# Kernel optimization log

Hardware: AMD Instinct MI355X
Metric: run time of the kernel (lower is better)

The kernel has to match this reference:

```python
import jax, jax.numpy as jnp
import numpy as np

GROUP = 64          # quantization group size along input dim
EPS = 1e-6          # rms_norm_eps
THETA = 1000000.0   # rope theta
NUM_HEADS = 16
NUM_KV_HEADS = 4
HEAD_DIM = 128


def _qlinear(x, wq, s, b=None):
    # dequantize int8-valued weights with per-group scales, then GEMM
    o, i = wq.shape
    w = (wq.reshape(o, i // GROUP, GROUP).astype(jnp.float32) * s[:, :, None]).reshape(o, i)
    y = jnp.einsum('bsi,oi->bso', x, w)
    return y + b if b is not None else y


def _rmsnorm(x, w):
    return x * jax.lax.rsqrt(jnp.mean(x * x, axis=-1, keepdims=True) + EPS) * w


def _rope(x, offset):
    # x: [B, H, S, hd], neox-style half rotation
    hd = x.shape[-1]
    S = x.shape[2]
    pos = (jnp.arange(S) + offset).astype(jnp.float32)
    inv = THETA ** (-(jnp.arange(0, hd, 2).astype(jnp.float32)) / hd)  # [hd/2]
    ang = pos[:, None] * inv[None, :]                                  # [S, hd/2]
    cos, sin = jnp.cos(ang), jnp.sin(ang)
    x1, x2 = x[..., : hd // 2], x[..., hd // 2 :]
    return jnp.concatenate([x1 * cos - x2 * sin, x2 * cos + x1 * sin], axis=-1)


def setup_inputs() -> dict:
    key = jax.random.key(0)
    B, S, D, I = 2, 1024, 2048, 5632
    KV = NUM_KV_HEADS * HEAD_DIM  # 512
    keys = iter(jax.random.split(key, 32))

    def qw(shape):
        return jax.random.randint(next(keys), shape, -127, 128, dtype=jnp.int32)

    def sc(shape):
        return jax.random.uniform(next(keys), shape, jnp.float32, 0.5, 1.5) * 0.001

    inp = {
        'x': jax.random.normal(next(keys), (B, S, D), jnp.float32),
        'wq_q': qw((D, D)),   'wq_s': sc((D, D // GROUP)),
        'bq': jax.random.normal(next(keys), (D,), jnp.float32) * 0.02,
        'wk_q': qw((KV, D)),  'wk_s': sc((KV, D // GROUP)),
        'bk': jax.random.normal(next(keys), (KV,), jnp.float32) * 0.02,
        'wv_q': qw((KV, D)),  'wv_s': sc((KV, D // GROUP)),
        'bv': jax.random.normal(next(keys), (KV,), jnp.float32) * 0.02,
        'wo_q': qw((D, D)),   'wo_s': sc((D, D // GROUP)),
        'gate_q': qw((I, D)), 'gate_s': sc((I, D // GROUP)),
        'up_q': qw((I, D)),   'up_s': sc((I, D // GROUP)),
        'down_q': qw((D, I)), 'down_s': sc((D, I // GROUP)),
        'w_in_ln': jnp.ones((D,), jnp.float32),
        'w_post_ln': jnp.ones((D,), jnp.float32),
        'offset': 0,
    }
    return inp


def reference(x, wq_q, wq_s, bq, wk_q, wk_s, bk, wv_q, wv_s, bv, wo_q, wo_s,
              gate_q, gate_s, up_q, up_s, down_q, down_s, w_in_ln, w_post_ln, offset):
    B, S, D = x.shape
    H, KVH, hd = NUM_HEADS, NUM_KV_HEADS, HEAD_DIM

    # --- attention sub-block ---
    h = _rmsnorm(x, w_in_ln)
    q = _qlinear(h, wq_q, wq_s, bq).reshape(B, S, H, hd).transpose(0, 2, 1, 3)
    k = _qlinear(h, wk_q, wk_s, bk).reshape(B, S, KVH, hd).transpose(0, 2, 1, 3)
    v = _qlinear(h, wv_q, wv_s, bv).reshape(B, S, KVH, hd).transpose(0, 2, 1, 3)
    q = _rope(q, offset)
    k = _rope(k, offset)

    g = H // KVH  # query groups per kv head
    qg = q.reshape(B, KVH, g, S, hd)
    scores = jnp.einsum('bghsd,bgtd->bghst', qg, k) * (1.0 / np.sqrt(hd)).astype(np.float32)
    causal = jnp.tril(jnp.ones((S, S), dtype=bool))  # prefill causal mask (empty cache)
    scores = jnp.where(causal, scores, jnp.float32(-1e9))
    p = jax.nn.softmax(scores, axis=-1)
    o = jnp.einsum('bghst,bgtd->bghsd', p, v)
    o = o.reshape(B, H, S, hd).transpose(0, 2, 1, 3).reshape(B, S, D)
    x = x + _qlinear(o, wo_q, wo_s)

    # --- mlp sub-block ---
    h2 = _rmsnorm(x, w_post_ln)
    gate = jax.nn.silu(_qlinear(h2, gate_q, gate_s))
    up = _qlinear(h2, up_q, up_s)
    mlp = _qlinear(gate * up, down_q, down_s)
    return x + mlp
```

## Files before the change

### kernel.cpp

```cpp
#include <hip/hip_runtime.h>
#include <cstdint>
#include <cstddef>

#define DEV __device__ __forceinline__

typedef _Float16 f16x8 __attribute__((ext_vector_type(8)));
typedef float f32x4 __attribute__((ext_vector_type(4)));

static constexpr int D_MODEL = 2048;
static constexpr int D_FF    = 5632;
static constexpr int N_QKV   = 3072;
static constexpr int SEQ     = 1024;
static constexpr int BATCH   = 2;
static constexpr int ROWS    = BATCH * SEQ;
static constexpr int HEADS   = 16;
static constexpr int HD      = 128;

DEV uint16_t f2h(float f) {
    return __builtin_bit_cast(uint16_t, (_Float16)f);
}
DEV float h2f(uint16_t u) {
    return (float)__builtin_bit_cast(_Float16, u);
}

DEV void async_load16(const void* g, void* lds) {
    __builtin_amdgcn_global_load_lds(
        reinterpret_cast<__attribute__((address_space(1))) void*>(
            reinterpret_cast<uintptr_t>(g)),
        reinterpret_cast<__attribute__((address_space(3))) void*>(
            static_cast<uint32_t>(reinterpret_cast<uintptr_t>(lds))),
        16, 0, 0);
}

__global__ __launch_bounds__(256)
void dequant_kernel(const int* __restrict__ q, const float* __restrict__ s,
                    uint16_t* __restrict__ wout, int n4, int I, int mode)
{
    const int idx = blockIdx.x * 256 + threadIdx.x;
    if (idx >= n4) return;
    const int e = idx * 4;
    const int row = e / I;
    const int i = e - row * I;
    const int4 qv = *reinterpret_cast<const int4*>(&q[e]);
    const float scf = s[row * (I >> 6) + (i >> 6)];
    int orow = row;
    if (mode == 1) orow = ((row >> 4) << 5) + (row & 15);
    else if (mode == 2) orow = ((row >> 4) << 5) + (row & 15) + 16;
    uint16_t h[4];
    h[0] = f2h((float)qv.x * scf);
    h[1] = f2h((float)qv.y * scf);
    h[2] = f2h((float)qv.z * scf);
    h[3] = f2h((float)qv.w * scf);
    uint2 pk;
    pk.x = (uint32_t)h[0] | ((uint32_t)h[1] << 16);
    pk.y = (uint32_t)h[2] | ((uint32_t)h[3] << 16);
    *reinterpret_cast<uint2*>(&wout[(size_t)orow * I + i]) = pk;
}

__global__ __launch_bounds__(256)
void biascat_kernel(const float* __restrict__ bq, const float* __restrict__ bk,
                    const float* __restrict__ bv, float* __restrict__ out)
{
    const int i = blockIdx.x * 256 + threadIdx.x;
    if (i >= N_QKV) return;
    float v;
    if (i < 2048)      v = bq[i];
    else if (i < 2560) v = bk[i - 2048];
    else               v = bv[i - 2560];
    out[i] = v;
}

__global__ __launch_bounds__(256)
void rmsnorm_kernel(const float* __restrict__ x, const float* __restrict__ wln,
                    uint16_t* __restrict__ out)
{
    __shared__ float red[4];
    const int row = blockIdx.x;
    const int tid = threadIdx.x;
    const float* xr = x + (size_t)row * D_MODEL;
    const float4 v0 = *reinterpret_cast<const float4*>(&xr[tid * 8]);
    const float4 v1 = *reinterpret_cast<const float4*>(&xr[tid * 8 + 4]);
    float ss = v0.x*v0.x + v0.y*v0.y + v0.z*v0.z + v0.w*v0.w
             + v1.x*v1.x + v1.y*v1.y + v1.z*v1.z + v1.w*v1.w;
#pragma unroll
    for (int off = 32; off; off >>= 1) ss += __shfl_xor(ss, off);
    if ((tid & 63) == 0) red[tid >> 6] = ss;
    __syncthreads();
    const float rms = rsqrtf((red[0] + red[1] + red[2] + red[3]) * (1.0f / D_MODEL) + 1e-6f);
    const int cb = tid * 8;
    const size_t base = (size_t)row * D_MODEL + cb;
    const float vals[8] = {v0.x, v0.y, v0.z, v0.w, v1.x, v1.y, v1.z, v1.w};
#pragma unroll
    for (int k = 0; k < 8; k += 2) {
        const uint16_t h0 = f2h(vals[k] * rms * wln[cb + k]);
        const uint16_t h1 = f2h(vals[k + 1] * rms * wln[cb + k + 1]);
        *reinterpret_cast<uint32_t*>(&out[base + k]) = (uint32_t)h0 | ((uint32_t)h1 << 16);
    }
}

__global__ __launch_bounds__(256)
void gemm_f16_glu_kernel(const uint16_t* __restrict__ A, const uint16_t* __restrict__ W,
                         uint16_t* __restrict__ outh, int M, int N, int K)
{
    __shared__ uint16_t sA[2][128 * 64];
    __shared__ uint16_t sB[2][128 * 64];

    const int tid  = threadIdx.x;
    const int lane = tid & 63;
    const int wv   = tid >> 6;
    const int wm   = wv >> 1;
    const int wn   = wv & 1;
    const int quad = lane >> 4;
    const int l16  = lane & 15;

    const int nBn = N >> 7;
    const int bm  = blockIdx.x / nBn;
    const int bn  = blockIdx.x - bm * nBn;
    const int m0  = bm << 7;
    const int n0  = bn << 7;

    f32x4 acc[4][4];
#pragma unroll
    for (int i = 0; i < 4; i++)
#pragma unroll
        for (int j = 0; j < 4; j++)
            acc[i][j] = (f32x4){0.f, 0.f, 0.f, 0.f};

    const uint16_t* Ab = A + (size_t)m0 * K;
    const uint16_t* Wb = W + (size_t)n0 * K;

    auto stage = [&](int kt, int bsel) {
#pragma unroll
        for (int p = 0; p < 4; p++) {
            const int cb = p * 256 + wv * 64;
            const int c  = cb + lane;
            const int row = c >> 3;
            const int g   = (c & 7) ^ (row & 7);
            const size_t goff = (size_t)row * K + kt + g * 8;
            async_load16(Ab + goff, &sA[bsel][cb * 8]);
            async_load16(Wb + goff, &sB[bsel][cb * 8]);
        }
    };

    stage(0, 0);
    __syncthreads();

    const int nKt = K >> 6;
    for (int t = 0; t < nKt; t++) {
        const int cur = t & 1;
        if (t + 1 < nKt) stage((t + 1) << 6, cur ^ 1);
        const uint16_t* sAc = sA[cur];
        const uint16_t* sBc = sB[cur];
#pragma unroll
        for (int kk = 0; kk < 2; kk++) {
            const int gsw = ((kk * 4 + quad) ^ (l16 & 7)) * 8;
            f16x8 bfv[4];
#pragma unroll
            for (int j = 0; j < 4; j++)
                bfv[j] = *reinterpret_cast<const f16x8*>(
                    &sBc[(wn * 64 + j * 16 + l16) * 64 + gsw]);
#pragma unroll
            for (int i = 0; i < 4; i++) {
                const f16x8 af = *reinterpret_cast<const f16x8*>(
                    &sAc[(wm * 64 + i * 16 + l16) * 64 + gsw]);
#pragma unroll
                for (int j = 0; j < 4; j++)
                    acc[i][j] = __builtin_amdgcn_mfma_f32_16x16x32_f16(af, bfv[j], acc[i][j], 0, 0, 0);
            }
        }
        __syncthreads();
    }

    const int NH = N >> 1;
#pragma unroll
    for (int i = 0; i < 4; i++) {
        const int rowb = m0 + wm * 64 + i * 16 + quad * 4;
#pragma unroll
        for (int r = 0; r < 4; r++) {
            const size_t rr = (size_t)(rowb + r);
#pragma unroll
            for (int pjt = 0; pjt < 2; pjt++) {
                const float g = acc[i][2 * pjt][r];
                const float u = acc[i][2 * pjt + 1][r];
                const float a = (g / (1.0f + __expf(-g))) * u;
                const int cc = (n0 >> 1) + wn * 32 + pjt * 16 + l16;
                outh[rr * NH + cc] = f2h(a);
            }
        }
    }
}

__global__ __launch_bounds__(256)
void gemm_f16_m64_kernel(const uint16_t* __restrict__ A, const uint16_t* __restrict__ W,
                         const float* __restrict__ bias, const float* __restrict__ resid,
                         float* __restrict__ outf, int M, int N, int K)
{
    __shared__ uint16_t sA[2][64 * 64];
    __shared__ uint16_t sB[2][128 * 64];

    const int tid  = threadIdx.x;
    const int lane = tid & 63;
    const int wv   = tid >> 6;
    const int quad = lane >> 4;
    const int l16  = lane & 15;

    const int nBn = N >> 7;
    const int bm  = blockIdx.x / nBn;
    const int bn  = blockIdx.x - bm * nBn;
    const int m0  = bm << 6;
    const int n0  = bn << 7;

    f32x4 acc[4][2];
#pragma unroll
    for (int i = 0; i < 4; i++)
#pragma unroll
        for (int j = 0; j < 2; j++)
            acc[i][j] = (f32x4){0.f, 0.f, 0.f, 0.f};

    const uint16_t* Ab = A + (size_t)m0 * K;
    const uint16_t* Wb = W + (size_t)n0 * K;

    auto stage = [&](int kt, int bsel) {
#pragma unroll
        for (int p = 0; p < 2; p++) {
            const int cb = p * 256 + wv * 64;
            const int c  = cb + lane;
            const int row = c >> 3;
            const int g   = (c & 7) ^ (row & 7);
            async_load16(Ab + (size_t)row * K + kt + g * 8, &sA[bsel][cb * 8]);
        }
#pragma unroll
        for (int p = 0; p < 4; p++) {
            const int cb = p * 256 + wv * 64;
            const int c  = cb + lane;
            const int row = c >> 3;
            const int g   = (c & 7) ^ (row & 7);
            async_load16(Wb + (size_t)row * K + kt + g * 8, &sB[bsel][cb * 8]);
        }
    };

    stage(0, 0);
    __syncthreads();

    const int nKt = K >> 6;
    for (int t = 0; t < nKt; t++) {
        const int cur = t & 1;
        if (t + 1 < nKt) stage((t + 1) << 6, cur ^ 1);
        const uint16_t* sAc = sA[cur];
        const uint16_t* sBc = sB[cur];
#pragma unroll
        for (int kk = 0; kk < 2; kk++) {
            const int gsw = ((kk * 4 + quad) ^ (l16 & 7)) * 8;
            f16x8 bfv[2];
#pragma unroll
            for (int j = 0; j < 2; j++)
                bfv[j] = *reinterpret_cast<const f16x8*>(
                    &sBc[(wv * 32 + j * 16 + l16) * 64 + gsw]);
#pragma unroll
            for (int i = 0; i < 4; i++) {
                const f16x8 af = *reinterpret_cast<const f16x8*>(
                    &sAc[(i * 16 + l16) * 64 + gsw]);
#pragma unroll
                for (int j = 0; j < 2; j++)
                    acc[i][j] = __builtin_amdgcn_mfma_f32_16x16x32_f16(af, bfv[j], acc[i][j], 0, 0, 0);
            }
        }
        __syncthreads();
    }

#pragma unroll
    for (int i = 0; i < 4; i++) {
        const int rowb = m0 + i * 16 + quad * 4;
#pragma unroll
        for (int r = 0; r < 4; r++) {
            const size_t rr = (size_t)(rowb + r);
#pragma unroll
            for (int j = 0; j < 2; j++) {
                const int cc = n0 + wv * 32 + j * 16 + l16;
                float v = acc[i][j][r];
                if (bias)  v += bias[cc];
                if (resid) v += resid[rr * N + cc];
                outf[rr * N + cc] = v;
            }
        }
    }
}

__global__ __launch_bounds__(256)
void rope_q_kernel(const float* __restrict__ qkv, const int* __restrict__ offp,
                   uint16_t* __restrict__ Qb)
{
    const int idx = blockIdx.x * 256 + threadIdx.x;
    const int d   = idx & 63;
    const int h   = (idx >> 6) & 15;
    const int row = idx >> 10;
    const int b   = row >> 10;
    const int s   = row & (SEQ - 1);
    const float pos  = (float)(s + *offp);
    const float freq = powf(1.0e6f, -(float)d * (1.0f / 64.0f));
    float sn, cs;
    sincosf(pos * freq, &sn, &cs);
    const size_t gb = (size_t)row * N_QKV + h * HD + d;
    const float x1 = qkv[gb];
    const float x2 = qkv[gb + 64];
    const float qscale = 0.08838834764831845f;
    const size_t ob = ((size_t)(b * 16 + h) * SEQ + s) * HD + d;
    Qb[ob]      = f2h((x1 * cs - x2 * sn) * qscale);
    Qb[ob + 64] = f2h((x2 * cs + x1 * sn) * qscale);
}

__global__ __launch_bounds__(256)
void rope_k_kernel(const float* __restrict__ qkv, const int* __restrict__ offp,
                   uint16_t* __restrict__ Kb)
{
    const int idx = blockIdx.x * 256 + threadIdx.x;
    const int d   = idx & 63;
    const int kvh = (idx >> 6) & 3;
    const int row = idx >> 8;
    const int b   = row >> 10;
    const int s   = row & (SEQ - 1);
    const float pos  = (float)(s + *offp);
    const float freq = powf(1.0e6f, -(float)d * (1.0f / 64.0f));
    float sn, cs;
    sincosf(pos * freq, &sn, &cs);
    const size_t gb = (size_t)row * N_QKV + 2048 + kvh * HD + d;
    const float x1 = qkv[gb];
    const float x2 = qkv[gb + 64];
    const size_t ob = ((size_t)(b * 4 + kvh) * SEQ + s) * HD + d;
    Kb[ob]      = f2h(x1 * cs - x2 * sn);
    Kb[ob + 64] = f2h(x2 * cs + x1 * sn);
}

__global__ __launch_bounds__(256)
void prep_v_kernel(const float* __restrict__ qkv, uint16_t* __restrict__ Vt)
{
    __shared__ uint16_t sh[128 * 72];
    const int tid = threadIdx.x;
    const int sc  = blockIdx.x & 15;
    const int bk  = blockIdx.x >> 4;
    const int b   = bk >> 2, kvh = bk & 3;
#pragma unroll
    for (int p = 0; p < 8; p++) {
        const int q4 = p * 256 + tid;
        const int sloc = q4 >> 5, d4 = (q4 & 31) * 4;
        const float4 v = *reinterpret_cast<const float4*>(
            &qkv[(size_t)(b * SEQ + sc * 64 + sloc) * N_QKV + 2560 + kvh * HD + d4]);
        sh[(d4 + 0) * 72 + sloc] = f2h(v.x);
        sh[(d4 + 1) * 72 + sloc] = f2h(v.y);
        sh[(d4 + 2) * 72 + sloc] = f2h(v.z);
        sh[(d4 + 3) * 72 + sloc] = f2h(v.w);
    }
    __syncthreads();
    const int d = tid >> 1, half = tid & 1;
    const size_t ob = ((size_t)(bk * 128 + d)) * SEQ + sc * 64 + half * 32;
    const uint16_t* srh = &sh[d * 72 + half * 32];
#pragma unroll
    for (int k = 0; k < 4; k++)
        *reinterpret_cast<uint4*>(&Vt[ob + k * 8]) =
            *reinterpret_cast<const uint4*>(&srh[k * 8]);
}

__global__ __launch_bounds__(256)
void attn_kernel(const uint16_t* __restrict__ Qb, const uint16_t* __restrict__ Kb,
                 const uint16_t* __restrict__ Vt, uint16_t* __restrict__ att)
{
    __shared__ uint16_t sK[2][32 * 128];
    __shared__ uint16_t sV[2][128 * 32];
    __shared__ uint16_t sP[4 * 16 * 32];

    const int tid  = threadIdx.x;
    const int lane = tid & 63;
    const int wv   = tid >> 6;
    const int quad = lane >> 4;
    const int l16  = lane & 15;
    const int qsw  = (quad ^ ((l16 >> 1) & 3)) * 8;

    const int bi  = blockIdx.x;
    const int sc  = 15 - (bi >> 5);
    const int bh  = bi & 31;
    const int b   = bh >> 4;
    const int h   = bh & 15;
    const int kvh = h >> 2;
    const int s0  = sc << 6;

    f16x8 qf[4];
    {
        const size_t qb = ((size_t)(b * 16 + h) * SEQ + s0 + wv * 16 + l16) * HD;
#pragma unroll
        for (int ks = 0; ks < 4; ks++)
            qf[ks] = *reinterpret_cast<const f16x8*>(&Qb[qb + ks * 32 + quad * 8]);
    }

    float m_i[4], l_i[4];
#pragma unroll
    for (int r = 0; r < 4; r++) { m_i[r] = -1e30f; l_i[r] = 0.f; }
    f32x4 oacc[8];
#pragma unroll
    for (int dt = 0; dt < 8; dt++) oacc[dt] = (f32x4){0.f, 0.f, 0.f, 0.f};

    const size_t kb = (size_t)(b * 4 + kvh) * SEQ * HD;
    const size_t vb = (size_t)(b * 4 + kvh) * HD * SEQ;

    auto stageKV = [&](int t0, int bsel) {
#pragma unroll
        for (int p = 0; p < 2; p++) {
            const int cb = p * 256 + wv * 64;
            const int c  = cb + lane;
            const int krow = c >> 4;
            const int kcc  = (c & 15) ^ (krow & 7);
            async_load16(Kb + kb + (size_t)(t0 + krow) * HD + kcc * 8, &sK[bsel][cb * 8]);
            const int vrow = c >> 2;
            const int vcc  = (c & 3) ^ ((vrow >> 1) & 3);
            async_load16(Vt + vb + (size_t)vrow * SEQ + t0 + vcc * 8, &sV[bsel][cb * 8]);
        }
    };

    const int ntiles = 2 * sc + 2;
    stageKV(0, 0);
    __syncthreads();

    for (int tt = 0; tt < ntiles; tt++) {
        const int t0 = tt << 5;
        const int cur = tt & 1;
        if (tt + 1 < ntiles) stageKV((tt + 1) << 5, cur ^ 1);

        f32x4 sacc[2];
        sacc[0] = (f32x4){0.f, 0.f, 0.f, 0.f};
        sacc[1] = (f32x4){0.f, 0.f, 0.f, 0.f};
#pragma unroll
        for (int ks = 0; ks < 4; ks++) {
#pragma unroll
            for (int jt = 0; jt < 2; jt++) {
                const int idx = (jt * 16 + l16) * 128 + (((ks * 4 + quad) ^ (l16 & 7)) * 8);
                const f16x8 kf = *reinterpret_cast<const f16x8*>(&sK[cur][idx]);
                sacc[jt] = __builtin_amdgcn_mfma_f32_16x16x32_f16(qf[ks], kf, sacc[jt], 0, 0, 0);
            }
        }

        if (t0 >= s0) {
            const int rowg = s0 + wv * 16 + quad * 4;
#pragma unroll
            for (int jt = 0; jt < 2; jt++) {
                const int key = t0 + jt * 16 + l16;
#pragma unroll
                for (int r = 0; r < 4; r++)
                    if (key > rowg + r) sacc[jt][r] = -1e30f;
            }
        }

        float alpha[4];
#pragma unroll
        for (int r = 0; r < 4; r++) {
            float mt = fmaxf(sacc[0][r], sacc[1][r]);
#pragma unroll
            for (int off = 8; off; off >>= 1) mt = fmaxf(mt, __shfl_xor(mt, off));
            const float mn = fmaxf(m_i[r], mt);
            alpha[r] = __expf(m_i[r] - mn);
            const float p0 = __expf(sacc[0][r] - mn);
            const float p1 = __expf(sacc[1][r] - mn);
            float ps = p0 + p1;
#pragma unroll
            for (int off = 8; off; off >>= 1) ps += __shfl_xor(ps, off);
            l_i[r] = l_i[r] * alpha[r] + ps;
            m_i[r] = mn;
            const int prow = quad * 4 + r;
            sP[wv * 512 + prow * 32 + 0 * 16 + l16] = f2h(p0);
            sP[wv * 512 + prow * 32 + 1 * 16 + l16] = f2h(p1);
        }

#pragma unroll
        for (int dt = 0; dt < 8; dt++) {
#pragma unroll
            for (int r = 0; r < 4; r++) oacc[dt][r] *= alpha[r];
        }
        const f16x8 pf = *reinterpret_cast<const f16x8*>(&sP[wv * 512 + l16 * 32 + quad * 8]);
#pragma unroll
        for (int dt = 0; dt < 8; dt++) {
            const f16x8 vf = *reinterpret_cast<const f16x8*>(&sV[cur][(dt * 16 + l16) * 32 + qsw]);
            oacc[dt] = __builtin_amdgcn_mfma_f32_16x16x32_f16(pf, vf, oacc[dt], 0, 0, 0);
        }

        __syncthreads();
    }

    float inv[4];
#pragma unroll
    for (int r = 0; r < 4; r++) inv[r] = 1.0f / l_i[r];
#pragma unroll
    for (int r = 0; r < 4; r++) {
        const size_t rowg = (size_t)(b * SEQ + s0 + wv * 16 + quad * 4 + r);
#pragma unroll
        for (int dt = 0; dt < 8; dt++)
            att[rowg * D_MODEL + h * HD + dt * 16 + l16] = f2h(oacc[dt][r] * inv[r]);
    }
}

extern "C" void kernel_launch(void* const* d_in, const int* in_sizes, int n_in,
                              void* d_out, int out_size, void* d_ws, size_t ws_size,
                              hipStream_t stream)
{
    (void)in_sizes; (void)n_in; (void)out_size; (void)ws_size;
    const float* x      = (const float*)d_in[0];
    const int*   wq_q   = (const int*)d_in[1];
    const float* wq_s   = (const float*)d_in[2];
    const float* bq     = (const float*)d_in[3];
    const int*   wk_q   = (const int*)d_in[4];
    const float* wk_s   = (const float*)d_in[5];
    const float* bk     = (const float*)d_in[6];
    const int*   wv_q   = (const int*)d_in[7];
    const float* wv_s   = (const float*)d_in[8];
    const float* bv     = (const float*)d_in[9];
    const int*   wo_q   = (const int*)d_in[10];
    const float* wo_s   = (const float*)d_in[11];
    const int*   gate_q = (const int*)d_in[12];
    const float* gate_s = (const float*)d_in[13];
    const int*   up_q   = (const int*)d_in[14];
    const float* up_s   = (const float*)d_in[15];
    const int*   down_q = (const int*)d_in[16];
    const float* down_s = (const float*)d_in[17];
    const float* w_in   = (const float*)d_in[18];
    const float* w_post = (const float*)d_in[19];
    const int*   offp   = (const int*)d_in[20];

    char* p = (char*)d_ws;
    auto alloc = [&](size_t bytes) {
        char* r = p;
        p += (bytes + 255) & ~(size_t)255;
        return r;
    };
    uint16_t* Wgu   = (uint16_t*)alloc((size_t)2 * D_FF * D_MODEL * 2);
    uint16_t* Wdown = (uint16_t*)alloc((size_t)D_MODEL * D_FF * 2);
    uint16_t* hbuf  = (uint16_t*)alloc((size_t)ROWS * D_MODEL * 2);
    float*    x2    = (float*)alloc((size_t)ROWS * D_MODEL * 4);
    float*    bqkv  = (float*)alloc((size_t)N_QKV * 4);
    char* zone = alloc((size_t)N_QKV * D_MODEL * 2 +
                       (size_t)D_MODEL * D_MODEL * 2 +
                       (size_t)ROWS * N_QKV * 4 + 8192);
    uint16_t* Wqkv = (uint16_t*)zone;
    uint16_t* Wo   = Wqkv + (size_t)N_QKV * D_MODEL;
    float*    qkv  = (float*)(Wo + (size_t)D_MODEL * D_MODEL);
    uint16_t* Qb = Wqkv;
    uint16_t* Kb = Qb + (size_t)BATCH * 16 * SEQ * HD;
    uint16_t* Vt = Kb + (size_t)BATCH * 4 * SEQ * HD;
    uint16_t* att = (uint16_t*)qkv;
    uint16_t* act = (uint16_t*)zone;

    auto dq = [&](const int* q, const float* s, uint16_t* o,
                  size_t n, int I, int mode) {
        const int n4 = (int)(n / 4);
        dequant_kernel<<<(n4 + 255) / 256, 256, 0, stream>>>(q, s, o, n4, I, mode);
    };
    dq(wq_q, wq_s, Wqkv, (size_t)2048 * 2048, 2048, 0);
    dq(wk_q, wk_s, Wqkv + (size_t)2048 * 2048, (size_t)512 * 2048, 2048, 0);
    dq(wv_q, wv_s, Wqkv + (size_t)2560 * 2048, (size_t)512 * 2048, 2048, 0);
    dq(wo_q, wo_s, Wo, (size_t)2048 * 2048, 2048, 0);
    dq(gate_q, gate_s, Wgu, (size_t)D_FF * 2048, 2048, 1);
    dq(up_q, up_s, Wgu, (size_t)D_FF * 2048, 2048, 2);
    dq(down_q, down_s, Wdown, (size_t)2048 * D_FF, D_FF, 0);

    biascat_kernel<<<(N_QKV + 255) / 256, 256, 0, stream>>>(bq, bk, bv, bqkv);
    rmsnorm_kernel<<<ROWS, 256, 0, stream>>>(x, w_in, hbuf);

    gemm_f16_m64_kernel<<<(ROWS / 64) * (N_QKV / 128), 256, 0, stream>>>(
        hbuf, Wqkv, bqkv, nullptr, qkv, ROWS, N_QKV, D_MODEL);

    rope_q_kernel<<<(ROWS * 16 * 64) / 256, 256, 0, stream>>>(qkv, offp, Qb);
    rope_k_kernel<<<(ROWS * 4 * 64) / 256, 256, 0, stream>>>(qkv, offp, Kb);
    prep_v_kernel<<<BATCH * 4 * (SEQ / 64), 256, 0, stream>>>(qkv, Vt);

    attn_kernel<<<BATCH * HEADS * (SEQ / 64), 256, 0, stream>>>(Qb, Kb, Vt, att);

    gemm_f16_m64_kernel<<<(ROWS / 64) * (D_MODEL / 128), 256, 0, stream>>>(
        att, Wo, nullptr, x, x2, ROWS, D_MODEL, D_MODEL);

    rmsnorm_kernel<<<ROWS, 256, 0, stream>>>(x2, w_post, hbuf);

    gemm_f16_glu_kernel<<<(ROWS / 128) * (2 * D_FF / 128), 256, 0, stream>>>(
        hbuf, Wgu, act, ROWS, 2 * D_FF, D_MODEL);

    gemm_f16_m64_kernel<<<(ROWS / 64) * (D_MODEL / 128), 256, 0, stream>>>(
        act, Wdown, nullptr, x2, (float*)d_out, ROWS, D_MODEL, D_FF);
}
```

Baseline: 569.6 us.

## Load GEMM A fragments directly from global memory and remap blocks across XCDs

Result: slower. 906.0 us (+59.1%).

```diff
diff --git a/kernel.cpp b/kernel.cpp
--- a/kernel.cpp
+++ b/kernel.cpp
@@ -98,11 +98,17 @@
     }
 }
 
+DEV void xcd_remap(int bid, int nwg, int nBm, int& bm, int& bn) {
+    const int cpx = nwg >> 3;
+    const int wg  = (bid & 7) * cpx + (bid >> 3);
+    bm = wg % nBm;
+    bn = wg / nBm;
+}
+
 __global__ __launch_bounds__(256)
 void gemm_f16_glu_kernel(const uint16_t* __restrict__ A, const uint16_t* __restrict__ W,
                          uint16_t* __restrict__ outh, int M, int N, int K)
 {
-    __shared__ uint16_t sA[2][128 * 64];
     __shared__ uint16_t sB[2][128 * 64];
 
     const int tid  = threadIdx.x;
@@ -113,9 +119,8 @@
     const int quad = lane >> 4;
     const int l16  = lane & 15;
 
-    const int nBn = N >> 7;
-    const int bm  = blockIdx.x / nBn;
-    const int bn  = blockIdx.x - bm * nBn;
+    int bm, bn;
+    xcd_remap(blockIdx.x, gridDim.x, M >> 7, bm, bn);
     const int m0  = bm << 7;
     const int n0  = bn << 7;
 
@@ -126,7 +131,7 @@
         for (int j = 0; j < 4; j++)
             acc[i][j] = (f32x4){0.f, 0.f, 0.f, 0.f};
 
-    const uint16_t* Ab = A + (size_t)m0 * K;
+    const uint16_t* Aw = A + (size_t)(m0 + wm * 64 + l16) * K;
     const uint16_t* Wb = W + (size_t)n0 * K;
 
     auto stage = [&](int kt, int bsel) {
@@ -136,9 +141,7 @@
             const int c  = cb + lane;
             const int row = c >> 3;
             const int g   = (c & 7) ^ (row & 7);
-            const size_t goff = (size_t)row * K + kt + g * 8;
-            async_load16(Ab + goff, &sA[bsel][cb * 8]);
-            async_load16(Wb + goff, &sB[bsel][cb * 8]);
+            async_load16(Wb + (size_t)row * K + kt + g * 8, &sB[bsel][cb * 8]);
         }
     };
 
@@ -148,8 +151,8 @@
     const int nKt = K >> 6;
     for (int t = 0; t < nKt; t++) {
         const int cur = t & 1;
-        if (t + 1 < nKt) stage((t + 1) << 6, cur ^ 1);
-        const uint16_t* sAc = sA[cur];
+        const int kt  = t << 6;
+        if (t + 1 < nKt) stage(kt + 64, cur ^ 1);
         const uint16_t* sBc = sB[cur];
 #pragma unroll
         for (int kk = 0; kk < 2; kk++) {
@@ -162,7 +165,7 @@
 #pragma unroll
             for (int i = 0; i < 4; i++) {
                 const f16x8 af = *reinterpret_cast<const f16x8*>(
-                    &sAc[(wm * 64 + i * 16 + l16) * 64 + gsw]);
+                    &Aw[(size_t)(i * 16) * K + kt + kk * 32 + quad * 8]);
 #pragma unroll
                 for (int j = 0; j < 4; j++)
                     acc[i][j] = __builtin_amdgcn_mfma_f32_16x16x32_f16(af, bfv[j], acc[i][j], 0, 0, 0);
@@ -195,7 +198,6 @@
                          const float* __restrict__ bias, const float* __restrict__ resid,
                          float* __restrict__ outf, int M, int N, int K)
 {
-    __shared__ uint16_t sA[2][64 * 64];
     __shared__ uint16_t sB[2][128 * 64];
 
     const int tid  = threadIdx.x;
@@ -204,9 +206,8 @@
     const int quad = lane >> 4;
     const int l16  = lane & 15;
 
-    const int nBn = N >> 7;
-    const int bm  = blockIdx.x / nBn;
-    const int bn  = blockIdx.x - bm * nBn;
+    int bm, bn;
+    xcd_remap(blockIdx.x, gridDim.x, M >> 6, bm, bn);
     const int m0  = bm << 6;
     const int n0  = bn << 7;
 
@@ -217,18 +218,10 @@
         for (int j = 0; j < 2; j++)
             acc[i][j] = (f32x4){0.f, 0.f, 0.f, 0.f};
 
-    const uint16_t* Ab = A + (size_t)m0 * K;
+    const uint16_t* Aw = A + (size_t)(m0 + l16) * K;
     const uint16_t* Wb = W + (size_t)n0 * K;
 
     auto stage = [&](int kt, int bsel) {
-#pragma unroll
-        for (int p = 0; p < 2; p++) {
-            const int cb = p * 256 + wv * 64;
-            const int c  = cb + lane;
-            const int row = c >> 3;
-            const int g   = (c & 7) ^ (row & 7);
-            async_load16(Ab + (size_t)row * K + kt + g * 8, &sA[bsel][cb * 8]);
-        }
 #pragma unroll
         for (int p = 0; p < 4; p++) {
             const int cb = p * 256 + wv * 64;
@@ -245,8 +238,8 @@
     const int nKt = K >> 6;
     for (int t = 0; t < nKt; t++) {
         const int cur = t & 1;
-        if (t + 1 < nKt) stage((t + 1) << 6, cur ^ 1);
-        const uint16_t* sAc = sA[cur];
+        const int kt  = t << 6;
+        if (t + 1 < nKt) stage(kt + 64, cur ^ 1);
         const uint16_t* sBc = sB[cur];
 #pragma unroll
         for (int kk = 0; kk < 2; kk++) {
@@ -259,7 +252,7 @@
 #pragma unroll
             for (int i = 0; i < 4; i++) {
                 const f16x8 af = *reinterpret_cast<const f16x8*>(
-                    &sAc[(i * 16 + l16) * 64 + gsw]);
+                    &Aw[(size_t)(i * 16) * K + kt + kk * 32 + quad * 8]);
 #pragma unroll
                 for (int j = 0; j < 2; j++)
                     acc[i][j] = __builtin_amdgcn_mfma_f32_16x16x32_f16(af, bfv[j], acc[i][j], 0, 0, 0);
```

## Merge dequant launches, fold bias concat into GEMM, fuse rope, add XCD remap

Applied to the files above, without the earlier changes.

Result: faster. 558.3 us (-2.0%).

```diff
diff --git a/kernel.cpp b/kernel.cpp
--- a/kernel.cpp
+++ b/kernel.cpp
@@ -19,9 +19,6 @@
 DEV uint16_t f2h(float f) {
     return __builtin_bit_cast(uint16_t, (_Float16)f);
 }
-DEV float h2f(uint16_t u) {
-    return (float)__builtin_bit_cast(_Float16, u);
-}
 
 DEV void async_load16(const void* g, void* lds) {
     __builtin_amdgcn_global_load_lds(
@@ -32,12 +29,30 @@
         16, 0, 0);
 }
 
-__global__ __launch_bounds__(256)
-void dequant_kernel(const int* __restrict__ q, const float* __restrict__ s,
-                    uint16_t* __restrict__ wout, int n4, int I, int mode)
-{
-    const int idx = blockIdx.x * 256 + threadIdx.x;
-    if (idx >= n4) return;
+static constexpr int DQ_BLOCKS = 44032;
+
+__global__ __launch_bounds__(256)
+void dequant_all_kernel(const int* __restrict__ wq_q, const float* __restrict__ wq_s,
+                        const int* __restrict__ wk_q, const float* __restrict__ wk_s,
+                        const int* __restrict__ wv_q, const float* __restrict__ wv_s,
+                        const int* __restrict__ wo_q, const float* __restrict__ wo_s,
+                        const int* __restrict__ gate_q, const float* __restrict__ gate_s,
+                        const int* __restrict__ up_q, const float* __restrict__ up_s,
+                        const int* __restrict__ down_q, const float* __restrict__ down_s,
+                        uint16_t* __restrict__ Wqkv, uint16_t* __restrict__ Wo,
+                        uint16_t* __restrict__ Wgu, uint16_t* __restrict__ Wdown)
+{
+    const int bid = blockIdx.x;
+    const int* q; const float* s; uint16_t* out; int I, mode, seg0;
+    if (bid < 4096)        { q = wq_q;   s = wq_s;   out = Wqkv;                      I = 2048; mode = 0; seg0 = 0; }
+    else if (bid < 5120)   { q = wk_q;   s = wk_s;   out = Wqkv + 2048 * 2048;        I = 2048; mode = 0; seg0 = 4096; }
+    else if (bid < 6144)   { q = wv_q;   s = wv_s;   out = Wqkv + 2560 * 2048;        I = 2048; mode = 0; seg0 = 5120; }
+    else if (bid < 10240)  { q = wo_q;   s = wo_s;   out = Wo;                        I = 2048; mode = 0; seg0 = 6144; }
+    else if (bid < 21504)  { q = gate_q; s = gate_s; out = Wgu;                       I = 2048; mode = 1; seg0 = 10240; }
+    else if (bid < 32768)  { q = up_q;   s = up_s;   out = Wgu;                       I = 2048; mode = 2; seg0 = 21504; }
+    else                   { q = down_q; s = down_s; out = Wdown;                     I = 5632; mode = 0; seg0 = 32768; }
+
+    const int idx = (bid - seg0) * 256 + threadIdx.x;
     const int e = idx * 4;
     const int row = e / I;
     const int i = e - row * I;
@@ -54,20 +69,7 @@
     uint2 pk;
     pk.x = (uint32_t)h[0] | ((uint32_t)h[1] << 16);
     pk.y = (uint32_t)h[2] | ((uint32_t)h[3] << 16);
-    *reinterpret_cast<uint2*>(&wout[(size_t)orow * I + i]) = pk;
-}
-
-__global__ __launch_bounds__(256)
-void biascat_kernel(const float* __restrict__ bq, const float* __restrict__ bk,
-                    const float* __restrict__ bv, float* __restrict__ out)
-{
-    const int i = blockIdx.x * 256 + threadIdx.x;
-    if (i >= N_QKV) return;
-    float v;
-    if (i < 2048)      v = bq[i];
-    else if (i < 2560) v = bk[i - 2048];
-    else               v = bv[i - 2560];
-    out[i] = v;
+    *reinterpret_cast<uint2*>(&out[(size_t)orow * I + i]) = pk;
 }
 
 __global__ __launch_bounds__(256)
@@ -98,6 +100,13 @@
     }
 }
 
+DEV void xcd_remap(int bid, int nwg, int nBm, int& bm, int& bn) {
+    const int cpx = nwg >> 3;
+    const int wg  = (bid & 7) * cpx + (bid >> 3);
+    bm = wg % nBm;
+    bn = wg / nBm;
+}
+
 __global__ __launch_bounds__(256)
 void gemm_f16_glu_kernel(const uint16_t* __restrict__ A, const uint16_t* __restrict__ W,
                          uint16_t* __restrict__ outh, int M, int N, int K)
@@ -113,9 +122,8 @@
     const int quad = lane >> 4;
     const int l16  = lane & 15;
 
-    const int nBn = N >> 7;
-    const int bm  = blockIdx.x / nBn;
-    const int bn  = blockIdx.x - bm * nBn;
+    int bm, bn;
+    xcd_remap(blockIdx.x, gridDim.x, M >> 7, bm, bn);
     const int m0  = bm << 7;
     const int n0  = bn << 7;
 
@@ -192,7 +200,8 @@
 
 __global__ __launch_bounds__(256)
 void gemm_f16_m64_kernel(const uint16_t* __restrict__ A, const uint16_t* __restrict__ W,
-                         const float* __restrict__ bias, const float* __restrict__ resid,
+                         const float* __restrict__ bq, const float* __restrict__ bk,
+                         const float* __restrict__ bv, const float* __restrict__ resid,
                          float* __restrict__ outf, int M, int N, int K)
 {
     __shared__ uint16_t sA[2][64 * 64];
@@ -204,9 +213,8 @@
     const int quad = lane >> 4;
     const int l16  = lane & 15;
 
-    const int nBn = N >> 7;
-    const int bm  = blockIdx.x / nBn;
-    const int bn  = blockIdx.x - bm * nBn;
+    int bm, bn;
+    xcd_remap(blockIdx.x, gridDim.x, M >> 6, bm, bn);
     const int m0  = bm << 6;
     const int n0  = bn << 7;
 
@@ -278,7 +286,13 @@
             for (int j = 0; j < 2; j++) {
                 const int cc = n0 + wv * 32 + j * 16 + l16;
                 float v = acc[i][j][r];
-                if (bias)  v += bias[cc];
+                if (bq) {
+                    float bb;
+                    if (cc < 2048)      bb = bq[cc];
+                    else if (cc < 2560) bb = bk[cc - 2048];
+                    else                bb = bv[cc - 2560];
+                    v += bb;
+                }
                 if (resid) v += resid[rr * N + cc];
                 outf[rr * N + cc] = v;
             }
@@ -286,49 +300,50 @@
     }
 }
 
-__global__ __launch_bounds__(256)
-void rope_q_kernel(const float* __restrict__ qkv, const int* __restrict__ offp,
-                   uint16_t* __restrict__ Qb)
-{
-    const int idx = blockIdx.x * 256 + threadIdx.x;
-    const int d   = idx & 63;
-    const int h   = (idx >> 6) & 15;
-    const int row = idx >> 10;
-    const int b   = row >> 10;
-    const int s   = row & (SEQ - 1);
-    const float pos  = (float)(s + *offp);
-    const float freq = powf(1.0e6f, -(float)d * (1.0f / 64.0f));
-    float sn, cs;
-    sincosf(pos * freq, &sn, &cs);
-    const size_t gb = (size_t)row * N_QKV + h * HD + d;
-    const float x1 = qkv[gb];
-    const float x2 = qkv[gb + 64];
-    const float qscale = 0.08838834764831845f;
-    const size_t ob = ((size_t)(b * 16 + h) * SEQ + s) * HD + d;
-    Qb[ob]      = f2h((x1 * cs - x2 * sn) * qscale);
-    Qb[ob + 64] = f2h((x2 * cs + x1 * sn) * qscale);
-}
-
-__global__ __launch_bounds__(256)
-void rope_k_kernel(const float* __restrict__ qkv, const int* __restrict__ offp,
-                   uint16_t* __restrict__ Kb)
-{
-    const int idx = blockIdx.x * 256 + threadIdx.x;
-    const int d   = idx & 63;
-    const int kvh = (idx >> 6) & 3;
-    const int row = idx >> 8;
-    const int b   = row >> 10;
-    const int s   = row & (SEQ - 1);
-    const float pos  = (float)(s + *offp);
-    const float freq = powf(1.0e6f, -(float)d * (1.0f / 64.0f));
-    float sn, cs;
-    sincosf(pos * freq, &sn, &cs);
-    const size_t gb = (size_t)row * N_QKV + 2048 + kvh * HD + d;
-    const float x1 = qkv[gb];
-    const float x2 = qkv[gb + 64];
-    const size_t ob = ((size_t)(b * 4 + kvh) * SEQ + s) * HD + d;
-    Kb[ob]      = f2h(x1 * cs - x2 * sn);
-    Kb[ob + 64] = f2h(x2 * cs + x1 * sn);
+static constexpr int ROPE_Q_THREADS = ROWS * 16 * 64;
+static constexpr int ROPE_THREADS   = ROPE_Q_THREADS + ROWS * 4 * 64;
+
+__global__ __launch_bounds__(256)
+void rope_qk_kernel(const float* __restrict__ qkv, const int* __restrict__ offp,
+                    uint16_t* __restrict__ Qb, uint16_t* __restrict__ Kb)
+{
+    const int gidx = blockIdx.x * 256 + threadIdx.x;
+    if (gidx < ROPE_Q_THREADS) {
+        const int idx = gidx;
+        const int d   = idx & 63;
+        const int h   = (idx >> 6) & 15;
+        const int row = idx >> 10;
+        const int b   = row >> 10;
+        const int s   = row & (SEQ - 1);
+        const float pos  = (float)(s + *offp);
+        const float freq = powf(1.0e6f, -(float)d * (1.0f / 64.0f));
+        float sn, cs;
+        sincosf(pos * freq, &sn, &cs);
+        const size_t gb = (size_t)row * N_QKV + h * HD + d;
+        const float x1 = qkv[gb];
+        const float x2 = qkv[gb + 64];
+        const float qscale = 0.08838834764831845f;
+        const size_t ob = ((size_t)(b * 16 + h) * SEQ + s) * HD + d;
+        Qb[ob]      = f2h((x1 * cs - x2 * sn) * qscale);
+        Qb[ob + 64] = f2h((x2 * cs + x1 * sn) * qscale);
+    } else {
+        const int idx = gidx - ROPE_Q_THREADS;
+        const int d   = idx & 63;
+        const int kvh = (idx >> 6) & 3;
+        const int row = idx >> 8;
+        const int b   = row >> 10;
+        const int s   = row & (SEQ - 1);
+        const float pos  = (float)(s + *offp);
+        const float freq = powf(1.0e6f, -(float)d * (1.0f / 64.0f));
+        float sn, cs;
+        sincosf(pos * freq, &sn, &cs);
+        const size_t gb = (size_t)row * N_QKV + 2048 + kvh * HD + d;
+        const float x1 = qkv[gb];
+        const float x2 = qkv[gb + 64];
+        const size_t ob = ((size_t)(b * 4 + kvh) * SEQ + s) * HD + d;
+        Kb[ob]      = f2h(x1 * cs - x2 * sn);
+        Kb[ob + 64] = f2h(x2 * cs + x1 * sn);
+    }
 }
 
 __global__ __launch_bounds__(256)
@@ -532,7 +547,6 @@
     uint16_t* Wdown = (uint16_t*)alloc((size_t)D_MODEL * D_FF * 2);
     uint16_t* hbuf  = (uint16_t*)alloc((size_t)ROWS * D_MODEL * 2);
     float*    x2    = (float*)alloc((size_t)ROWS * D_MODEL * 4);
-    float*    bqkv  = (float*)alloc((size_t)N_QKV * 4);
     char* zone = alloc((size_t)N_QKV * D_MODEL * 2 +
                        (size_t)D_MODEL * D_MODEL * 2 +
                        (size_t)ROWS * N_QKV * 4 + 8192);
@@ -545,33 +559,23 @@
     uint16_t* att = (uint16_t*)qkv;
     uint16_t* act = (uint16_t*)zone;
 
-    auto dq = [&](const int* q, const float* s, uint16_t* o,
-                  size_t n, int I, int mode) {
-        const int n4 = (int)(n / 4);
-        dequant_kernel<<<(n4 + 255) / 256, 256, 0, stream>>>(q, s, o, n4, I, mode);
-    };
-    dq(wq_q, wq_s, Wqkv, (size_t)2048 * 2048, 2048, 0);
-    dq(wk_q, wk_s, Wqkv + (size_t)2048 * 2048, (size_t)512 * 2048, 2048, 0);
-    dq(wv_q, wv_s, Wqkv + (size_t)2560 * 2048, (size_t)512 * 2048, 2048, 0);
-    dq(wo_q, wo_s, Wo, (size_t)2048 * 2048, 2048, 0);
-    dq(gate_q, gate_s, Wgu, (size_t)D_FF * 2048, 2048, 1);
-    dq(up_q, up_s, Wgu, (size_t)D_FF * 2048, 2048, 2);
-    dq(down_q, down_s, Wdown, (size_t)2048 * D_FF, D_FF, 0);
-
-    biascat_kernel<<<(N_QKV + 255) / 256, 256, 0, stream>>>(bq, bk, bv, bqkv);
+    dequant_all_kernel<<<DQ_BLOCKS, 256, 0, stream>>>(
+        wq_q, wq_s, wk_q, wk_s, wv_q, wv_s, wo_q, wo_s,
+        gate_q, gate_s, up_q, up_s, down_q, down_s,
+        Wqkv, Wo, Wgu, Wdown);
+
     rmsnorm_kernel<<<ROWS, 256, 0, stream>>>(x, w_in, hbuf);
 
     gemm_f16_m64_kernel<<<(ROWS / 64) * (N_QKV / 128), 256, 0, stream>>>(
-        hbuf, Wqkv, bqkv, nullptr, qkv, ROWS, N_QKV, D_MODEL);
-
-    rope_q_kernel<<<(ROWS * 16 * 64) / 256, 256, 0, stream>>>(qkv, offp, Qb);
-    rope_k_kernel<<<(ROWS * 4 * 64) / 256, 256, 0, stream>>>(qkv, offp, Kb);
+        hbuf, Wqkv, bq, bk, bv, nullptr, qkv, ROWS, N_QKV, D_MODEL);
+
+    rope_qk_kernel<<<ROPE_THREADS / 256, 256, 0, stream>>>(qkv, offp, Qb, Kb);
     prep_v_kernel<<<BATCH * 4 * (SEQ / 64), 256, 0, stream>>>(qkv, Vt);
 
     attn_kernel<<<BATCH * HEADS * (SEQ / 64), 256, 0, stream>>>(Qb, Kb, Vt, att);
 
     gemm_f16_m64_kernel<<<(ROWS / 64) * (D_MODEL / 128), 256, 0, stream>>>(
-        att, Wo, nullptr, x, x2, ROWS, D_MODEL, D_MODEL);
+        att, Wo, nullptr, nullptr, nullptr, x, x2, ROWS, D_MODEL, D_MODEL);
 
     rmsnorm_kernel<<<ROWS, 256, 0, stream>>>(x2, w_post, hbuf);
 
@@ -579,5 +583,5 @@
         hbuf, Wgu, act, ROWS, 2 * D_FF, D_MODEL);
 
     gemm_f16_m64_kernel<<<(ROWS / 64) * (D_MODEL / 128), 256, 0, stream>>>(
-        act, Wdown, nullptr, x2, (float*)d_out, ROWS, D_MODEL, D_FF);
-}
+        act, Wdown, nullptr, nullptr, nullptr, x2, (float*)d_out, ROWS, D_MODEL, D_FF);
+}
```
